# Performance work log

Measured on AMD Instinct MI355X. Metric: run time of the kernel, lower is better.

## Reference

```python
import jax, jax.numpy as jnp
import numpy as np

D_MODEL = 1024
NUM_HEADS = 16
HEAD_DIM = D_MODEL // NUM_HEADS
B, S = 2, 2048


def setup_inputs() -> dict:
    key = jax.random.key(0)
    ks = jax.random.split(key, 5)
    x = jax.random.normal(ks[0], (B, S, D_MODEL), dtype=jnp.float32)
    # nn.Linear weights are [out_features, in_features]
    Wq = jax.random.normal(ks[1], (D_MODEL, D_MODEL), dtype=jnp.float32) / np.sqrt(D_MODEL)
    Wk = jax.random.normal(ks[2], (HEAD_DIM, D_MODEL), dtype=jnp.float32) / np.sqrt(D_MODEL)
    Wv = jax.random.normal(ks[3], (HEAD_DIM, D_MODEL), dtype=jnp.float32) / np.sqrt(D_MODEL)
    Wo = jax.random.normal(ks[4], (D_MODEL, D_MODEL), dtype=jnp.float32) / np.sqrt(D_MODEL)
    # causal mask, broadcastable to [B, H, S, S]; mask==0 positions get -inf
    mask = jnp.tril(jnp.ones((S, S), dtype=bool))[None, None]
    return {"x": x, "Wq": Wq, "Wk": Wk, "Wv": Wv, "Wo": Wo, "mask": mask}


def reference(x, Wq, Wk, Wv, Wo, mask):
    Bsz, Sl, D = x.shape
    H, hd = NUM_HEADS, HEAD_DIM
    q = (x @ Wq.T).reshape(Bsz, Sl, H, hd)          # [B,S,H,hd]
    k = x @ Wk.T                                    # [B,S,hd] (single shared KV head)
    v = x @ Wv.T                                    # [B,S,hd]
    scale = 1.0 / np.sqrt(hd).astype(np.float32)
    # scores: [B,H,S,S] — full O(n^2) matrix, as in the original module
    scores = jnp.einsum('bshd,btd->bhst', q, k) * scale
    scores = jnp.where(mask, scores, -jnp.inf)
    attn = jax.nn.softmax(scores, axis=-1)
    out = jnp.einsum('bhst,btd->bshd', attn, v).reshape(Bsz, Sl, D)
    return out @ Wo.T
```

## Files before the change

### kernel.cpp

```cpp
#include <hip/hip_runtime.h>
#include <hip/hip_bf16.h>
#include <math.h>

#define BB 2
#define SS 2048
#define DD 1024
#define NH 16
#define HD 64
#define MM (BB * SS)

typedef __hip_bfloat16 bf16;
typedef __bf16 bf16_t;
typedef __attribute__((ext_vector_type(8))) __bf16 bf16x8;
typedef __attribute__((ext_vector_type(4))) __bf16 bf16x4;
typedef __attribute__((ext_vector_type(4))) float floatx4;

__global__ void detect_dtype(const unsigned int* __restrict__ x, int* __restrict__ flag) {
    const int tid = threadIdx.x;
    int good = 0;
    for (int i = tid; i < 256; i += 64) {
        unsigned int bits = (x[i] & 0xFFFFu) << 16;
        float v = __uint_as_float(bits);
        float av = fabsf(v);
        if (av == 0.f || (av >= 9.5367431640625e-7f && av <= 64.f)) good++;
    }
#pragma unroll
    for (int s = 1; s < 64; s <<= 1) good += __shfl_xor(good, s);
    if (tid == 0) *flag = (good >= 240) ? 0 : 1;
}

#define BK 32
#define KP 40

__device__ __forceinline__ bf16x4 cvt4(float4 v) {
    bf16x4 o;
    o[0] = (bf16_t)v.x; o[1] = (bf16_t)v.y; o[2] = (bf16_t)v.z; o[3] = (bf16_t)v.w;
    return o;
}

__global__ __launch_bounds__(256) void proj_qkv(const void* __restrict__ X,
                                                const void* __restrict__ Wq,
                                                const void* __restrict__ Wk,
                                                const void* __restrict__ Wv,
                                                bf16_t* __restrict__ QA,
                                                bf16_t* __restrict__ Kp,
                                                bf16_t* __restrict__ VpT,
                                                const int* __restrict__ flag) {
    const int f = *flag;

    __shared__ bf16_t As[128 * KP];
    __shared__ bf16_t Ws[128 * KP];

    const int tid = threadIdx.x;
    const int wave = tid >> 6, lane = tid & 63;
    const int lo = lane & 15, quad = lane >> 4;
    const int wr = wave >> 1, wc = wave & 1;
    const int cb = blockIdx.x;
    const int rowBase = blockIdx.y * 128;

    floatx4 acc[4][4];
#pragma unroll
    for (int i = 0; i < 4; i++)
#pragma unroll
        for (int j = 0; j < 4; j++) acc[i][j] = (floatx4){0.f, 0.f, 0.f, 0.f};

    if (f) {
        const int rA = tid >> 3, sg = tid & 7;
        const float* wrow[4];
        const float* arow[4];
#pragma unroll
        for (int p = 0; p < 4; p++) {
            int row = rA + 32 * p;
            arow[p] = (const float*)X + (size_t)(rowBase + row) * DD;
            if (cb < 8)        wrow[p] = (const float*)Wq + (size_t)(cb * 128 + row) * DD;
            else if (row < 64) wrow[p] = (const float*)Wk + (size_t)row * DD;
            else               wrow[p] = (const float*)Wv + (size_t)(row - 64) * DD;
        }
        float4 aR[4], wR[4];
#pragma unroll
        for (int p = 0; p < 4; p++) {
            aR[p] = *(const float4*)(arow[p] + sg * 4);
            wR[p] = *(const float4*)(wrow[p] + sg * 4);
        }
        for (int k0 = 0; k0 < DD; k0 += BK) {
            __syncthreads();
#pragma unroll
            for (int p = 0; p < 4; p++) {
                *(bf16x4*)&As[(rA + 32 * p) * KP + sg * 4] = cvt4(aR[p]);
                *(bf16x4*)&Ws[(rA + 32 * p) * KP + sg * 4] = cvt4(wR[p]);
            }
            __syncthreads();
            if (k0 + BK < DD) {
#pragma unroll
                for (int p = 0; p < 4; p++) {
                    aR[p] = *(const float4*)(arow[p] + k0 + BK + sg * 4);
                    wR[p] = *(const float4*)(wrow[p] + k0 + BK + sg * 4);
                }
            }
            bf16x8 afr[4], bfr[4];
#pragma unroll
            for (int i = 0; i < 4; i++)
                afr[i] = *(const bf16x8*)&As[(wr * 64 + i * 16 + lo) * KP + quad * 8];
#pragma unroll
            for (int j = 0; j < 4; j++)
                bfr[j] = *(const bf16x8*)&Ws[(wc * 64 + j * 16 + lo) * KP + quad * 8];
#pragma unroll
            for (int i = 0; i < 4; i++)
#pragma unroll
                for (int j = 0; j < 4; j++)
                    acc[i][j] = __builtin_amdgcn_mfma_f32_16x16x32_bf16(afr[i], bfr[j], acc[i][j], 0, 0, 0);
        }
    } else {
        const int rA = tid >> 2, sg = tid & 3;
        const bf16_t* arow[2];
        const bf16_t* wrow[2];
#pragma unroll
        for (int p = 0; p < 2; p++) {
            int row = rA + 64 * p;
            arow[p] = (const bf16_t*)X + (size_t)(rowBase + row) * DD;
            if (cb < 8)        wrow[p] = (const bf16_t*)Wq + (size_t)(cb * 128 + row) * DD;
            else if (row < 64) wrow[p] = (const bf16_t*)Wk + (size_t)row * DD;
            else               wrow[p] = (const bf16_t*)Wv + (size_t)(row - 64) * DD;
        }
        bf16x8 aR[2], wR[2];
#pragma unroll
        for (int p = 0; p < 2; p++) {
            aR[p] = *(const bf16x8*)(arow[p] + sg * 8);
            wR[p] = *(const bf16x8*)(wrow[p] + sg * 8);
        }
        for (int k0 = 0; k0 < DD; k0 += BK) {
            __syncthreads();
#pragma unroll
            for (int p = 0; p < 2; p++) {
                *(bf16x8*)&As[(rA + 64 * p) * KP + sg * 8] = aR[p];
                *(bf16x8*)&Ws[(rA + 64 * p) * KP + sg * 8] = wR[p];
            }
            __syncthreads();
            if (k0 + BK < DD) {
#pragma unroll
                for (int p = 0; p < 2; p++) {
                    aR[p] = *(const bf16x8*)(arow[p] + k0 + BK + sg * 8);
                    wR[p] = *(const bf16x8*)(wrow[p] + k0 + BK + sg * 8);
                }
            }
            bf16x8 afr[4], bfr[4];
#pragma unroll
            for (int i = 0; i < 4; i++)
                afr[i] = *(const bf16x8*)&As[(wr * 64 + i * 16 + lo) * KP + quad * 8];
#pragma unroll
            for (int j = 0; j < 4; j++)
                bfr[j] = *(const bf16x8*)&Ws[(wc * 64 + j * 16 + lo) * KP + quad * 8];
#pragma unroll
            for (int i = 0; i < 4; i++)
#pragma unroll
                for (int j = 0; j < 4; j++)
                    acc[i][j] = __builtin_amdgcn_mfma_f32_16x16x32_bf16(afr[i], bfr[j], acc[i][j], 0, 0, 0);
        }
    }

#pragma unroll
    for (int i = 0; i < 4; i++)
#pragma unroll
        for (int j = 0; j < 4; j++)
#pragma unroll
            for (int reg = 0; reg < 4; reg++) {
                int row = rowBase + wr * 64 + i * 16 + quad * 4 + reg;
                int col = wc * 64 + j * 16 + lo;
                bf16_t val = (bf16_t)acc[i][j][reg];
                if (cb < 8)         QA[(size_t)row * DD + cb * 128 + col] = val;
                else if (col < 64)  Kp[(size_t)row * HD + col] = val;
                else {
                    int d = col - 64;
                    VpT[((size_t)(row >> 11) * HD + d) * SS + (row & (SS - 1))] = val;
                }
            }
}

__global__ __launch_bounds__(256) void proj_o(const bf16_t* __restrict__ AO,
                                              const void* __restrict__ Wo,
                                              void* __restrict__ Cout,
                                              const int* __restrict__ flag) {
    const int f = *flag;

    __shared__ bf16_t As[128 * KP];
    __shared__ bf16_t Ws[128 * KP];

    const int tid = threadIdx.x;
    const int wave = tid >> 6, lane = tid & 63;
    const int lo = lane & 15, quad = lane >> 4;
    const int wr = wave >> 1, wc = wave & 1;
    const int colBase = blockIdx.x * 128;
    const int rowBase = blockIdx.y * 128;

    floatx4 acc[4][4];
#pragma unroll
    for (int i = 0; i < 4; i++)
#pragma unroll
        for (int j = 0; j < 4; j++) acc[i][j] = (floatx4){0.f, 0.f, 0.f, 0.f};

    const int rA = tid >> 2, sgA = tid & 3;
    const bf16_t* arow[2] = {AO + (size_t)(rowBase + rA) * DD,
                             AO + (size_t)(rowBase + rA + 64) * DD};
    bf16x8 aR[2];
#pragma unroll
    for (int p = 0; p < 2; p++) aR[p] = *(const bf16x8*)(arow[p] + sgA * 8);

    if (f) {
        const int rW = tid >> 3, sgW = tid & 7;
        const float* wrow[4];
#pragma unroll
        for (int p = 0; p < 4; p++)
            wrow[p] = (const float*)Wo + (size_t)(colBase + rW + 32 * p) * DD;
        float4 wR[4];
#pragma unroll
        for (int p = 0; p < 4; p++) wR[p] = *(const float4*)(wrow[p] + sgW * 4);

        for (int k0 = 0; k0 < DD; k0 += BK) {
            __syncthreads();
#pragma unroll
            for (int p = 0; p < 2; p++)
                *(bf16x8*)&As[(rA + 64 * p) * KP + sgA * 8] = aR[p];
#pragma unroll
            for (int p = 0; p < 4; p++)
                *(bf16x4*)&Ws[(rW + 32 * p) * KP + sgW * 4] = cvt4(wR[p]);
            __syncthreads();
            if (k0 + BK < DD) {
#pragma unroll
                for (int p = 0; p < 2; p++)
                    aR[p] = *(const bf16x8*)(arow[p] + k0 + BK + sgA * 8);
#pragma unroll
                for (int p = 0; p < 4; p++)
                    wR[p] = *(const float4*)(wrow[p] + k0 + BK + sgW * 4);
            }
            bf16x8 afr[4], bfr[4];
#pragma unroll
            for (int i = 0; i < 4; i++)
                afr[i] = *(const bf16x8*)&As[(wr * 64 + i * 16 + lo) * KP + quad * 8];
#pragma unroll
            for (int j = 0; j < 4; j++)
                bfr[j] = *(const bf16x8*)&Ws[(wc * 64 + j * 16 + lo) * KP + quad * 8];
#pragma unroll
            for (int i = 0; i < 4; i++)
#pragma unroll
                for (int j = 0; j < 4; j++)
                    acc[i][j] = __builtin_amdgcn_mfma_f32_16x16x32_bf16(afr[i], bfr[j], acc[i][j], 0, 0, 0);
        }
    } else {
        const int rW = tid >> 2, sgW = tid & 3;
        const bf16_t* wrow[2];
#pragma unroll
        for (int p = 0; p < 2; p++)
            wrow[p] = (const bf16_t*)Wo + (size_t)(colBase + rW + 64 * p) * DD;
        bf16x8 wR[2];
#pragma unroll
        for (int p = 0; p < 2; p++) wR[p] = *(const bf16x8*)(wrow[p] + sgW * 8);

        for (int k0 = 0; k0 < DD; k0 += BK) {
            __syncthreads();
#pragma unroll
            for (int p = 0; p < 2; p++) {
                *(bf16x8*)&As[(rA + 64 * p) * KP + sgA * 8] = aR[p];
                *(bf16x8*)&Ws[(rW + 64 * p) * KP + sgW * 8] = wR[p];
            }
            __syncthreads();
            if (k0 + BK < DD) {
#pragma unroll
                for (int p = 0; p < 2; p++) {
                    aR[p] = *(const bf16x8*)(arow[p] + k0 + BK + sgA * 8);
                    wR[p] = *(const bf16x8*)(wrow[p] + k0 + BK + sgW * 8);
                }
            }
            bf16x8 afr[4], bfr[4];
#pragma unroll
            for (int i = 0; i < 4; i++)
                afr[i] = *(const bf16x8*)&As[(wr * 64 + i * 16 + lo) * KP + quad * 8];
#pragma unroll
            for (int j = 0; j < 4; j++)
                bfr[j] = *(const bf16x8*)&Ws[(wc * 64 + j * 16 + lo) * KP + quad * 8];
#pragma unroll
            for (int i = 0; i < 4; i++)
#pragma unroll
                for (int j = 0; j < 4; j++)
                    acc[i][j] = __builtin_amdgcn_mfma_f32_16x16x32_bf16(afr[i], bfr[j], acc[i][j], 0, 0, 0);
        }
    }

#pragma unroll
    for (int i = 0; i < 4; i++)
#pragma unroll
        for (int j = 0; j < 4; j++)
#pragma unroll
            for (int reg = 0; reg < 4; reg++) {
                int row = rowBase + wr * 64 + i * 16 + quad * 4 + reg;
                int col = colBase + wc * 64 + j * 16 + lo;
                size_t idx = (size_t)row * DD + col;
                if (f) ((float*)Cout)[idx] = acc[i][j][reg];
                else   ((bf16_t*)Cout)[idx] = (bf16_t)acc[i][j][reg];
            }
}

#define PSTR 40
#define ALOG2E 0.18033688011112042f

__global__ __launch_bounds__(256) void attn_mfma(const bf16_t* Q,
                                                 const bf16_t* __restrict__ K,
                                                 const bf16_t* __restrict__ Vt,
                                                 bf16_t* O) {
    const int h = blockIdx.y, b = blockIdx.z;
    const int tid = threadIdx.x;
    const int wq = tid >> 6, lane = tid & 63;
    const int lo = lane & 15, quad = lane >> 4;
    const int x = blockIdx.x;
    const int qt = (wq & 1) ? (31 + (wq >> 1) * 32 - x) : ((wq >> 1) * 32 + x);
    const int q0 = qt * 32;

    __shared__ bf16_t Ps[4][32 * PSTR];
    bf16_t* Pw = Ps[wq];

    bf16x8 qf[2][2];
#pragma unroll
    for (int s = 0; s < 2; s++)
#pragma unroll
        for (int hf = 0; hf < 2; hf++)
            qf[s][hf] = *(const bf16x8*)(Q + ((size_t)(b * SS + q0 + s * 16 + lo)) * DD +
                                         h * HD + hf * 32 + quad * 8);

    floatx4 Oacc[2][4];
    float m_i[2], l_i[2];
#pragma unroll
    for (int s = 0; s < 2; s++) {
#pragma unroll
        for (int dt = 0; dt < 4; dt++) Oacc[s][dt] = (floatx4){0.f, 0.f, 0.f, 0.f};
        m_i[s] = -1e30f; l_i[s] = 0.f;
    }

    const bf16_t* Kb = K + (size_t)b * SS * HD;
    const bf16_t* Vb = Vt + (size_t)b * HD * SS;

    bf16x8 kf[2][2];
#pragma unroll
    for (int kt = 0; kt < 2; kt++)
#pragma unroll
        for (int hf = 0; hf < 2; hf++)
            kf[kt][hf] = *(const bf16x8*)(Kb + (size_t)(kt * 16 + lo) * HD + hf * 32 + quad * 8);

    for (int it = 0; it <= qt; it++) {
        const int t0 = it * 32;

        bf16x8 vf[4];
#pragma unroll
        for (int dt = 0; dt < 4; dt++)
            vf[dt] = *(const bf16x8*)(Vb + (size_t)(dt * 16 + lo) * SS + t0 + quad * 8);

        bf16x8 kn[2][2];
        if (it < qt) {
#pragma unroll
            for (int kt = 0; kt < 2; kt++)
#pragma unroll
                for (int hf = 0; hf < 2; hf++)
                    kn[kt][hf] = *(const bf16x8*)(Kb + (size_t)(t0 + 32 + kt * 16 + lo) * HD +
                                                  hf * 32 + quad * 8);
        }

        floatx4 st[2][2];
#pragma unroll
        for (int s = 0; s < 2; s++)
#pragma unroll
            for (int kt = 0; kt < 2; kt++) {
                floatx4 z = (floatx4){0.f, 0.f, 0.f, 0.f};
                z = __builtin_amdgcn_mfma_f32_16x16x32_bf16(kf[kt][0], qf[s][0], z, 0, 0, 0);
                z = __builtin_amdgcn_mfma_f32_16x16x32_bf16(kf[kt][1], qf[s][1], z, 0, 0, 0);
                st[s][kt] = z;
            }

        if (it == qt) {
#pragma unroll
            for (int s = 0; s < 2; s++) {
                int q = q0 + s * 16 + lo;
#pragma unroll
                for (int kt = 0; kt < 2; kt++)
#pragma unroll
                    for (int reg = 0; reg < 4; reg++)
                        if (t0 + kt * 16 + quad * 4 + reg > q) st[s][kt][reg] = -1e30f;
            }
        }

#pragma unroll
        for (int s = 0; s < 2; s++) {
            float mx = fmaxf(fmaxf(fmaxf(st[s][0][0], st[s][0][1]), fmaxf(st[s][0][2], st[s][0][3])),
                             fmaxf(fmaxf(st[s][1][0], st[s][1][1]), fmaxf(st[s][1][2], st[s][1][3])));
            mx = fmaxf(mx, __shfl_xor(mx, 16));
            mx = fmaxf(mx, __shfl_xor(mx, 32));
            float mn = fmaxf(m_i[s], mx);
            float al = exp2f((m_i[s] - mn) * ALOG2E);
            m_i[s] = mn;
            float mnA = mn * ALOG2E;
            float p[2][4];
#pragma unroll
            for (int kt = 0; kt < 2; kt++)
#pragma unroll
                for (int reg = 0; reg < 4; reg++)
                    p[kt][reg] = exp2f(st[s][kt][reg] * ALOG2E - mnA);
            float rs = ((p[0][0] + p[0][1]) + (p[0][2] + p[0][3])) +
                       ((p[1][0] + p[1][1]) + (p[1][2] + p[1][3]));
            rs += __shfl_xor(rs, 16);
            rs += __shfl_xor(rs, 32);
            l_i[s] = l_i[s] * al + rs;
#pragma unroll
            for (int kt = 0; kt < 2; kt++) {
                bf16x4 pk;
#pragma unroll
                for (int reg = 0; reg < 4; reg++) pk[reg] = (bf16_t)p[kt][reg];
                *(bf16x4*)&Pw[(s * 16 + lo) * PSTR + kt * 16 + quad * 4] = pk;
            }
#pragma unroll
            for (int dt = 0; dt < 4; dt++) Oacc[s][dt] *= al;
        }

        asm volatile("s_waitcnt lgkmcnt(0)" ::: "memory");

        bf16x8 pb[2];
#pragma unroll
        for (int s = 0; s < 2; s++)
            pb[s] = *(const bf16x8*)&Pw[(s * 16 + lo) * PSTR + quad * 8];
#pragma unroll
        for (int s = 0; s < 2; s++)
#pragma unroll
            for (int dt = 0; dt < 4; dt++)
                Oacc[s][dt] = __builtin_amdgcn_mfma_f32_16x16x32_bf16(vf[dt], pb[s], Oacc[s][dt], 0, 0, 0);

#pragma unroll
        for (int kt = 0; kt < 2; kt++)
#pragma unroll
            for (int hf = 0; hf < 2; hf++) kf[kt][hf] = kn[kt][hf];
    }

#pragma unroll
    for (int s = 0; s < 2; s++) {
        float inv = 1.f / l_i[s];
        bf16_t* Orow = O + ((size_t)(b * SS + q0 + s * 16 + lo)) * DD + h * HD;
#pragma unroll
        for (int dt = 0; dt < 4; dt++) {
            bf16x4 ov;
#pragma unroll
            for (int reg = 0; reg < 4; reg++) ov[reg] = (bf16_t)(Oacc[s][dt][reg] * inv);
            *(bf16x4*)&Orow[dt * 16 + quad * 4] = ov;
        }
    }
}

extern "C" void kernel_launch(void* const* d_in, const int* in_sizes, int n_in,
                              void* d_out, int out_size, void* d_ws, size_t ws_size,
                              hipStream_t stream) {
    const void* x  = d_in[0];
    const void* Wq = d_in[1];
    const void* Wk = d_in[2];
    const void* Wv = d_in[3];
    const void* Wo = d_in[4];

    char* ws = (char*)d_ws;
    int* flag = (int*)ws;
    bf16_t* QA  = (bf16_t*)(ws + 256);
    bf16_t* Kp  = QA + (size_t)MM * DD;
    bf16_t* VpT = Kp + (size_t)MM * HD;

    detect_dtype<<<1, 64, 0, stream>>>((const unsigned int*)x, flag);

    proj_qkv<<<dim3(9, MM / 128), dim3(256), 0, stream>>>(x, Wq, Wk, Wv, QA, Kp, VpT, flag);

    attn_mfma<<<dim3(SS / 32 / 4, NH, BB), dim3(256), 0, stream>>>(QA, Kp, VpT, QA);

    proj_o<<<dim3(DD / 128, MM / 128), dim3(256), 0, stream>>>(QA, Wo, d_out, flag);
}
```

Measured before the change: 226.1 us.

## Split attention KV range across wave pairs and shrink GEMM tiles for more blocks

The attention kernel now gives each pair of waves one query tile and splits its causal KV range in half. The two partial softmax states are merged through shared memory, which doubles the grid and balances work per wave. The projection GEMMs move from 128x128 to 128x64 output tiles so they launch twice as many blocks, which helps fill the CUs. The cost is lower data reuse per block in the GEMMs, extra shared memory in attention, and a block-wide sync for the merge.

Measured after the change: 210.7 us. 6.8% less time.

```diff
diff --git a/kernel.cpp b/kernel.cpp
--- a/kernel.cpp
+++ b/kernel.cpp
@@ -49,63 +49,65 @@
     const int f = *flag;
 
     __shared__ bf16_t As[128 * KP];
-    __shared__ bf16_t Ws[128 * KP];
+    __shared__ bf16_t Ws[64 * KP];
 
     const int tid = threadIdx.x;
     const int wave = tid >> 6, lane = tid & 63;
     const int lo = lane & 15, quad = lane >> 4;
-    const int wr = wave >> 1, wc = wave & 1;
+    const int rb = wave * 32;
     const int cb = blockIdx.x;
     const int rowBase = blockIdx.y * 128;
 
-    floatx4 acc[4][4];
-#pragma unroll
-    for (int i = 0; i < 4; i++)
+    floatx4 acc[2][4];
+#pragma unroll
+    for (int i = 0; i < 2; i++)
 #pragma unroll
         for (int j = 0; j < 4; j++) acc[i][j] = (floatx4){0.f, 0.f, 0.f, 0.f};
 
     if (f) {
         const int rA = tid >> 3, sg = tid & 7;
-        const float* wrow[4];
         const float* arow[4];
-#pragma unroll
-        for (int p = 0; p < 4; p++) {
+        const float* wrow[2];
+#pragma unroll
+        for (int p = 0; p < 4; p++)
+            arow[p] = (const float*)X + (size_t)(rowBase + rA + 32 * p) * DD;
+#pragma unroll
+        for (int p = 0; p < 2; p++) {
             int row = rA + 32 * p;
-            arow[p] = (const float*)X + (size_t)(rowBase + row) * DD;
-            if (cb < 8)        wrow[p] = (const float*)Wq + (size_t)(cb * 128 + row) * DD;
-            else if (row < 64) wrow[p] = (const float*)Wk + (size_t)row * DD;
-            else               wrow[p] = (const float*)Wv + (size_t)(row - 64) * DD;
-        }
-        float4 aR[4], wR[4];
-#pragma unroll
-        for (int p = 0; p < 4; p++) {
-            aR[p] = *(const float4*)(arow[p] + sg * 4);
-            wR[p] = *(const float4*)(wrow[p] + sg * 4);
-        }
+            if (cb < 16)       wrow[p] = (const float*)Wq + (size_t)(cb * 64 + row) * DD;
+            else if (cb == 16) wrow[p] = (const float*)Wk + (size_t)row * DD;
+            else               wrow[p] = (const float*)Wv + (size_t)row * DD;
+        }
+        float4 aR[4], wR[2];
+#pragma unroll
+        for (int p = 0; p < 4; p++) aR[p] = *(const float4*)(arow[p] + sg * 4);
+#pragma unroll
+        for (int p = 0; p < 2; p++) wR[p] = *(const float4*)(wrow[p] + sg * 4);
+
         for (int k0 = 0; k0 < DD; k0 += BK) {
             __syncthreads();
 #pragma unroll
-            for (int p = 0; p < 4; p++) {
+            for (int p = 0; p < 4; p++)
                 *(bf16x4*)&As[(rA + 32 * p) * KP + sg * 4] = cvt4(aR[p]);
+#pragma unroll
+            for (int p = 0; p < 2; p++)
                 *(bf16x4*)&Ws[(rA + 32 * p) * KP + sg * 4] = cvt4(wR[p]);
-            }
             __syncthreads();
             if (k0 + BK < DD) {
 #pragma unroll
-                for (int p = 0; p < 4; p++) {
-                    aR[p] = *(const float4*)(arow[p] + k0 + BK + sg * 4);
-                    wR[p] = *(const float4*)(wrow[p] + k0 + BK + sg * 4);
-                }
-            }
-            bf16x8 afr[4], bfr[4];
-#pragma unroll
-            for (int i = 0; i < 4; i++)
-                afr[i] = *(const bf16x8*)&As[(wr * 64 + i * 16 + lo) * KP + quad * 8];
+                for (int p = 0; p < 4; p++) aR[p] = *(const float4*)(arow[p] + k0 + BK + sg * 4);
+#pragma unroll
+                for (int p = 0; p < 2; p++) wR[p] = *(const float4*)(wrow[p] + k0 + BK + sg * 4);
+            }
+            bf16x8 afr[2], bfr[4];
+#pragma unroll
+            for (int i = 0; i < 2; i++)
+                afr[i] = *(const bf16x8*)&As[(rb + i * 16 + lo) * KP + quad * 8];
 #pragma unroll
             for (int j = 0; j < 4; j++)
-                bfr[j] = *(const bf16x8*)&Ws[(wc * 64 + j * 16 + lo) * KP + quad * 8];
-#pragma unroll
-            for (int i = 0; i < 4; i++)
+                bfr[j] = *(const bf16x8*)&Ws[(j * 16 + lo) * KP + quad * 8];
+#pragma unroll
+            for (int i = 0; i < 2; i++)
 #pragma unroll
                 for (int j = 0; j < 4; j++)
                     acc[i][j] = __builtin_amdgcn_mfma_f32_16x16x32_bf16(afr[i], bfr[j], acc[i][j], 0, 0, 0);
@@ -113,45 +115,39 @@
     } else {
         const int rA = tid >> 2, sg = tid & 3;
         const bf16_t* arow[2];
-        const bf16_t* wrow[2];
-#pragma unroll
-        for (int p = 0; p < 2; p++) {
-            int row = rA + 64 * p;
-            arow[p] = (const bf16_t*)X + (size_t)(rowBase + row) * DD;
-            if (cb < 8)        wrow[p] = (const bf16_t*)Wq + (size_t)(cb * 128 + row) * DD;
-            else if (row < 64) wrow[p] = (const bf16_t*)Wk + (size_t)row * DD;
-            else               wrow[p] = (const bf16_t*)Wv + (size_t)(row - 64) * DD;
-        }
-        bf16x8 aR[2], wR[2];
-#pragma unroll
-        for (int p = 0; p < 2; p++) {
-            aR[p] = *(const bf16x8*)(arow[p] + sg * 8);
-            wR[p] = *(const bf16x8*)(wrow[p] + sg * 8);
-        }
+        const bf16_t* wrow;
+#pragma unroll
+        for (int p = 0; p < 2; p++)
+            arow[p] = (const bf16_t*)X + (size_t)(rowBase + rA + 64 * p) * DD;
+        if (cb < 16)       wrow = (const bf16_t*)Wq + (size_t)(cb * 64 + rA) * DD;
+        else if (cb == 16) wrow = (const bf16_t*)Wk + (size_t)rA * DD;
+        else               wrow = (const bf16_t*)Wv + (size_t)rA * DD;
+        bf16x8 aR[2], wR;
+#pragma unroll
+        for (int p = 0; p < 2; p++) aR[p] = *(const bf16x8*)(arow[p] + sg * 8);
+        wR = *(const bf16x8*)(wrow + sg * 8);
+
         for (int k0 = 0; k0 < DD; k0 += BK) {
             __syncthreads();
 #pragma unroll
-            for (int p = 0; p < 2; p++) {
+            for (int p = 0; p < 2; p++)
                 *(bf16x8*)&As[(rA + 64 * p) * KP + sg * 8] = aR[p];
-                *(bf16x8*)&Ws[(rA + 64 * p) * KP + sg * 8] = wR[p];
-            }
+            *(bf16x8*)&Ws[rA * KP + sg * 8] = wR;
             __syncthreads();
             if (k0 + BK < DD) {
 #pragma unroll
-                for (int p = 0; p < 2; p++) {
-                    aR[p] = *(const bf16x8*)(arow[p] + k0 + BK + sg * 8);
-                    wR[p] = *(const bf16x8*)(wrow[p] + k0 + BK + sg * 8);
-                }
-            }
-            bf16x8 afr[4], bfr[4];
-#pragma unroll
-            for (int i = 0; i < 4; i++)
-                afr[i] = *(const bf16x8*)&As[(wr * 64 + i * 16 + lo) * KP + quad * 8];
+                for (int p = 0; p < 2; p++) aR[p] = *(const bf16x8*)(arow[p] + k0 + BK + sg * 8);
+                wR = *(const bf16x8*)(wrow + k0 + BK + sg * 8);
+            }
+            bf16x8 afr[2], bfr[4];
+#pragma unroll
+            for (int i = 0; i < 2; i++)
+                afr[i] = *(const bf16x8*)&As[(rb + i * 16 + lo) * KP + quad * 8];
 #pragma unroll
             for (int j = 0; j < 4; j++)
-                bfr[j] = *(const bf16x8*)&Ws[(wc * 64 + j * 16 + lo) * KP + quad * 8];
-#pragma unroll
-            for (int i = 0; i < 4; i++)
+                bfr[j] = *(const bf16x8*)&Ws[(j * 16 + lo) * KP + quad * 8];
+#pragma unroll
+            for (int i = 0; i < 2; i++)
 #pragma unroll
                 for (int j = 0; j < 4; j++)
                     acc[i][j] = __builtin_amdgcn_mfma_f32_16x16x32_bf16(afr[i], bfr[j], acc[i][j], 0, 0, 0);
@@ -159,20 +155,17 @@
     }
 
 #pragma unroll
-    for (int i = 0; i < 4; i++)
+    for (int i = 0; i < 2; i++)
 #pragma unroll
         for (int j = 0; j < 4; j++)
 #pragma unroll
             for (int reg = 0; reg < 4; reg++) {
-                int row = rowBase + wr * 64 + i * 16 + quad * 4 + reg;
-                int col = wc * 64 + j * 16 + lo;
+                int row = rowBase + rb + i * 16 + quad * 4 + reg;
+                int col = j * 16 + lo;
                 bf16_t val = (bf16_t)acc[i][j][reg];
-                if (cb < 8)         QA[(size_t)row * DD + cb * 128 + col] = val;
-                else if (col < 64)  Kp[(size_t)row * HD + col] = val;
-                else {
-                    int d = col - 64;
-                    VpT[((size_t)(row >> 11) * HD + d) * SS + (row & (SS - 1))] = val;
-                }
+                if (cb < 16)       QA[(size_t)row * DD + cb * 64 + col] = val;
+                else if (cb == 16) Kp[(size_t)row * HD + col] = val;
+                else               VpT[((size_t)(row >> 11) * HD + col) * SS + (row & (SS - 1))] = val;
             }
 }
 
@@ -183,102 +176,91 @@
     const int f = *flag;
 
     __shared__ bf16_t As[128 * KP];
-    __shared__ bf16_t Ws[128 * KP];
+    __shared__ bf16_t Ws[64 * KP];
 
     const int tid = threadIdx.x;
     const int wave = tid >> 6, lane = tid & 63;
     const int lo = lane & 15, quad = lane >> 4;
-    const int wr = wave >> 1, wc = wave & 1;
-    const int colBase = blockIdx.x * 128;
+    const int rb = wave * 32;
+    const int colBase = blockIdx.x * 64;
     const int rowBase = blockIdx.y * 128;
 
-    floatx4 acc[4][4];
-#pragma unroll
-    for (int i = 0; i < 4; i++)
+    floatx4 acc[2][4];
+#pragma unroll
+    for (int i = 0; i < 2; i++)
 #pragma unroll
         for (int j = 0; j < 4; j++) acc[i][j] = (floatx4){0.f, 0.f, 0.f, 0.f};
 
-    const int rA = tid >> 2, sgA = tid & 3;
-    const bf16_t* arow[2] = {AO + (size_t)(rowBase + rA) * DD,
-                             AO + (size_t)(rowBase + rA + 64) * DD};
+    const int rA2 = tid >> 2, sgA = tid & 3;
+    const bf16_t* arow[2] = {AO + (size_t)(rowBase + rA2) * DD,
+                             AO + (size_t)(rowBase + rA2 + 64) * DD};
     bf16x8 aR[2];
 #pragma unroll
     for (int p = 0; p < 2; p++) aR[p] = *(const bf16x8*)(arow[p] + sgA * 8);
 
     if (f) {
         const int rW = tid >> 3, sgW = tid & 7;
-        const float* wrow[4];
-#pragma unroll
-        for (int p = 0; p < 4; p++)
+        const float* wrow[2];
+#pragma unroll
+        for (int p = 0; p < 2; p++)
             wrow[p] = (const float*)Wo + (size_t)(colBase + rW + 32 * p) * DD;
-        float4 wR[4];
-#pragma unroll
-        for (int p = 0; p < 4; p++) wR[p] = *(const float4*)(wrow[p] + sgW * 4);
+        float4 wR[2];
+#pragma unroll
+        for (int p = 0; p < 2; p++) wR[p] = *(const float4*)(wrow[p] + sgW * 4);
 
         for (int k0 = 0; k0 < DD; k0 += BK) {
             __syncthreads();
 #pragma unroll
             for (int p = 0; p < 2; p++)
-                *(bf16x8*)&As[(rA + 64 * p) * KP + sgA * 8] = aR[p];
-#pragma unroll
-            for (int p = 0; p < 4; p++)
+                *(bf16x8*)&As[(rA2 + 64 * p) * KP + sgA * 8] = aR[p];
+#pragma unroll
+            for (int p = 0; p < 2; p++)
                 *(bf16x4*)&Ws[(rW + 32 * p) * KP + sgW * 4] = cvt4(wR[p]);
             __syncthreads();
             if (k0 + BK < DD) {
 #pragma unroll
-                for (int p = 0; p < 2; p++)
-                    aR[p] = *(const bf16x8*)(arow[p] + k0 + BK + sgA * 8);
-#pragma unroll
-                for (int p = 0; p < 4; p++)
-                    wR[p] = *(const float4*)(wrow[p] + k0 + BK + sgW * 4);
-            }
-            bf16x8 afr[4], bfr[4];
-#pragma unroll
-            for (int i = 0; i < 4; i++)
-                afr[i] = *(const bf16x8*)&As[(wr * 64 + i * 16 + lo) * KP + quad * 8];
+                for (int p = 0; p < 2; p++) aR[p] = *(const bf16x8*)(arow[p] + k0 + BK + sgA * 8);
+#pragma unroll
+                for (int p = 0; p < 2; p++) wR[p] = *(const float4*)(wrow[p] + k0 + BK + sgW * 4);
+            }
+            bf16x8 afr[2], bfr[4];
+#pragma unroll
+            for (int i = 0; i < 2; i++)
+                afr[i] = *(const bf16x8*)&As[(rb + i * 16 + lo) * KP + quad * 8];
 #pragma unroll
             for (int j = 0; j < 4; j++)
-                bfr[j] = *(const bf16x8*)&Ws[(wc * 64 + j * 16 + lo) * KP + quad * 8];
-#pragma unroll
-            for (int i = 0; i < 4; i++)
+                bfr[j] = *(const bf16x8*)&Ws[(j * 16 + lo) * KP + quad * 8];
+#pragma unroll
+            for (int i = 0; i < 2; i++)
 #pragma unroll
                 for (int j = 0; j < 4; j++)
                     acc[i][j] = __builtin_amdgcn_mfma_f32_16x16x32_bf16(afr[i], bfr[j], acc[i][j], 0, 0, 0);
         }
     } else {
-        const int rW = tid >> 2, sgW = tid & 3;
-        const bf16_t* wrow[2];
-#pragma unroll
-        for (int p = 0; p < 2; p++)
-            wrow[p] = (const bf16_t*)Wo + (size_t)(colBase + rW + 64 * p) * DD;
-        bf16x8 wR[2];
-#pragma unroll
-        for (int p = 0; p < 2; p++) wR[p] = *(const bf16x8*)(wrow[p] + sgW * 8);
+        const bf16_t* wrow = (const bf16_t*)Wo + (size_t)(colBase + rA2) * DD;
+        bf16x8 wR = *(const bf16x8*)(wrow + sgA * 8);
 
         for (int k0 = 0; k0 < DD; k0 += BK) {
             __syncthreads();
 #pragma unroll
-            for (int p = 0; p < 2; p++) {
-                *(bf16x8*)&As[(rA + 64 * p) * KP + sgA * 8] = aR[p];
-                *(bf16x8*)&Ws[(rW + 64 * p) * KP + sgW * 8] = wR[p];
-            }
+            for (int p = 0; p < 2; p++)
+                *(bf16x8*)&As[(rA2 + 64 * p) * KP + sgA * 8] = aR[p];
+            *(bf16x8*)&Ws[rA2 * KP + sgA * 8] = wR;
             __syncthreads();
             if (k0 + BK < DD) {
 #pragma unroll
-                for (int p = 0; p < 2; p++) {
-                    aR[p] = *(const bf16x8*)(arow[p] + k0 + BK + sgA * 8);
-                    wR[p] = *(const bf16x8*)(wrow[p] + k0 + BK + sgW * 8);
-                }
-            }
-            bf16x8 afr[4], bfr[4];
-#pragma unroll
-            for (int i = 0; i < 4; i++)
-                afr[i] = *(const bf16x8*)&As[(wr * 64 + i * 16 + lo) * KP + quad * 8];
+                for (int p = 0; p < 2; p++) aR[p] = *(const bf16x8*)(arow[p] + k0 + BK + sgA * 8);
+                wR = *(const bf16x8*)(wrow + k0 + BK + sgA * 8);
+            }
+            bf16x8 afr[2], bfr[4];
+#pragma unroll
+            for (int i = 0; i < 2; i++)
+                afr[i] = *(const bf16x8*)&As[(rb + i * 16 + lo) * KP + quad * 8];
 #pragma unroll
             for (int j = 0; j < 4; j++)
-                bfr[j] = *(const bf16x8*)&Ws[(wc * 64 + j * 16 + lo) * KP + quad * 8];
-#pragma unroll
-            for (int i = 0; i < 4; i++)
+                bfr[j] = *(const bf16x8*)&Ws[(j * 16 + lo) * KP + quad * 8];
+#pragma unroll
+            for (int i = 0; i < 2; i++)
 #pragma unroll
                 for (int j = 0; j < 4; j++)
                     acc[i][j] = __builtin_amdgcn_mfma_f32_16x16x32_bf16(afr[i], bfr[j], acc[i][j], 0, 0, 0);
@@ -286,13 +268,13 @@
     }
 
 #pragma unroll
-    for (int i = 0; i < 4; i++)
+    for (int i = 0; i < 2; i++)
 #pragma unroll
         for (int j = 0; j < 4; j++)
 #pragma unroll
             for (int reg = 0; reg < 4; reg++) {
-                int row = rowBase + wr * 64 + i * 16 + quad * 4 + reg;
-                int col = colBase + wc * 64 + j * 16 + lo;
+                int row = rowBase + rb + i * 16 + quad * 4 + reg;
+                int col = colBase + j * 16 + lo;
                 size_t idx = (size_t)row * DD + col;
                 if (f) ((float*)Cout)[idx] = acc[i][j][reg];
                 else   ((bf16_t*)Cout)[idx] = (bf16_t)acc[i][j][reg];
@@ -302,19 +284,27 @@
 #define PSTR 40
 #define ALOG2E 0.18033688011112042f
 
-__global__ __launch_bounds__(256) void attn_mfma(const bf16_t* Q,
-                                                 const bf16_t* __restrict__ K,
-                                                 const bf16_t* __restrict__ Vt,
-                                                 bf16_t* O) {
+__global__ __launch_bounds__(256, 4) void attn_mfma(const bf16_t* Q,
+                                                    const bf16_t* __restrict__ K,
+                                                    const bf16_t* __restrict__ Vt,
+                                                    bf16_t* O) {
     const int h = blockIdx.y, b = blockIdx.z;
     const int tid = threadIdx.x;
     const int wq = tid >> 6, lane = tid & 63;
     const int lo = lane & 15, quad = lane >> 4;
     const int x = blockIdx.x;
-    const int qt = (wq & 1) ? (31 + (wq >> 1) * 32 - x) : ((wq >> 1) * 32 + x);
+    const int pr = wq >> 1;
+    const int hh = wq & 1;
+    const int qt = pr ? (63 - x) : x;
     const int q0 = qt * 32;
+    const int nt = qt + 1;
+    const int nt0 = nt >> 1;
+    const int itS = hh ? nt0 : 0;
+    const int itE = hh ? nt : nt0;
 
     __shared__ bf16_t Ps[4][32 * PSTR];
+    __shared__ float MrgO[2][32][64];
+    __shared__ float MrgML[2][2][2][16];
     bf16_t* Pw = Ps[wq];
 
     bf16x8 qf[2][2];
@@ -337,114 +327,142 @@
     const bf16_t* Kb = K + (size_t)b * SS * HD;
     const bf16_t* Vb = Vt + (size_t)b * HD * SS;
 
-    bf16x8 kf[2][2];
-#pragma unroll
-    for (int kt = 0; kt < 2; kt++)
-#pragma unroll
-        for (int hf = 0; hf < 2; hf++)
-            kf[kt][hf] = *(const bf16x8*)(Kb + (size_t)(kt * 16 + lo) * HD + hf * 32 + quad * 8);
-
-    for (int it = 0; it <= qt; it++) {
-        const int t0 = it * 32;
-
-        bf16x8 vf[4];
-#pragma unroll
-        for (int dt = 0; dt < 4; dt++)
-            vf[dt] = *(const bf16x8*)(Vb + (size_t)(dt * 16 + lo) * SS + t0 + quad * 8);
-
-        bf16x8 kn[2][2];
-        if (it < qt) {
+    if (itS < itE) {
+        bf16x8 kf[2][2];
+#pragma unroll
+        for (int kt = 0; kt < 2; kt++)
+#pragma unroll
+            for (int hf = 0; hf < 2; hf++)
+                kf[kt][hf] = *(const bf16x8*)(Kb + (size_t)(itS * 32 + kt * 16 + lo) * HD +
+                                              hf * 32 + quad * 8);
+
+        for (int it = itS; it < itE; it++) {
+            const int t0 = it * 32;
+
+            bf16x8 vf[4];
+#pragma unroll
+            for (int dt = 0; dt < 4; dt++)
+                vf[dt] = *(const bf16x8*)(Vb + (size_t)(dt * 16 + lo) * SS + t0 + quad * 8);
+
+            bf16x8 kn[2][2];
+            if (it + 1 < itE) {
+#pragma unroll
+                for (int kt = 0; kt < 2; kt++)
+#pragma unroll
+                    for (int hf = 0; hf < 2; hf++)
+                        kn[kt][hf] = *(const bf16x8*)(Kb + (size_t)(t0 + 32 + kt * 16 + lo) * HD +
+                                                      hf * 32 + quad * 8);
+            }
+
+            floatx4 st[2][2];
+#pragma unroll
+            for (int s = 0; s < 2; s++)
+#pragma unroll
+                for (int kt = 0; kt < 2; kt++) {
+                    floatx4 z = (floatx4){0.f, 0.f, 0.f, 0.f};
+                    z = __builtin_amdgcn_mfma_f32_16x16x32_bf16(kf[kt][0], qf[s][0], z, 0, 0, 0);
+                    z = __builtin_amdgcn_mfma_f32_16x16x32_bf16(kf[kt][1], qf[s][1], z, 0, 0, 0);
+                    st[s][kt] = z;
+                }
+
+            if (it == qt) {
+#pragma unroll
+                for (int s = 0; s < 2; s++) {
+                    int q = q0 + s * 16 + lo;
+#pragma unroll
+                    for (int kt = 0; kt < 2; kt++)
+#pragma unroll
+                        for (int reg = 0; reg < 4; reg++)
+                            if (t0 + kt * 16 + quad * 4 + reg > q) st[s][kt][reg] = -1e30f;
+                }
+            }
+
+#pragma unroll
+            for (int s = 0; s < 2; s++) {
+                float mx = fmaxf(fmaxf(fmaxf(st[s][0][0], st[s][0][1]), fmaxf(st[s][0][2], st[s][0][3])),
+                                 fmaxf(fmaxf(st[s][1][0], st[s][1][1]), fmaxf(st[s][1][2], st[s][1][3])));
+                mx = fmaxf(mx, __shfl_xor(mx, 16));
+                mx = fmaxf(mx, __shfl_xor(mx, 32));
+                float mn = fmaxf(m_i[s], mx);
+                float al = exp2f((m_i[s] - mn) * ALOG2E);
+                m_i[s] = mn;
+                float mnA = mn * ALOG2E;
+                float p[2][4];
+#pragma unroll
+                for (int kt = 0; kt < 2; kt++)
+#pragma unroll
+                    for (int reg = 0; reg < 4; reg++)
+                        p[kt][reg] = exp2f(st[s][kt][reg] * ALOG2E - mnA);
+                float rs = ((p[0][0] + p[0][1]) + (p[0][2] + p[0][3])) +
+                           ((p[1][0] + p[1][1]) + (p[1][2] + p[1][3]));
+                rs += __shfl_xor(rs, 16);
+                rs += __shfl_xor(rs, 32);
+                l_i[s] = l_i[s] * al + rs;
+#pragma unroll
+                for (int kt = 0; kt < 2; kt++) {
+                    bf16x4 pk;
+#pragma unroll
+                    for (int reg = 0; reg < 4; reg++) pk[reg] = (bf16_t)p[kt][reg];
+                    *(bf16x4*)&Pw[(s * 16 + lo) * PSTR + kt * 16 + quad * 4] = pk;
+                }
+#pragma unroll
+                for (int dt = 0; dt < 4; dt++) Oacc[s][dt] *= al;
+            }
+
+            asm volatile("s_waitcnt lgkmcnt(0)" ::: "memory");
+
+            bf16x8 pb[2];
+#pragma unroll
+            for (int s = 0; s < 2; s++)
+                pb[s] = *(const bf16x8*)&Pw[(s * 16 + lo) * PSTR + quad * 8];
+#pragma unroll
+            for (int s = 0; s < 2; s++)
+#pragma unroll
+                for (int dt = 0; dt < 4; dt++)
+                    Oacc[s][dt] = __builtin_amdgcn_mfma_f32_16x16x32_bf16(vf[dt], pb[s], Oacc[s][dt], 0, 0, 0);
+
 #pragma unroll
             for (int kt = 0; kt < 2; kt++)
 #pragma unroll
-                for (int hf = 0; hf < 2; hf++)
-                    kn[kt][hf] = *(const bf16x8*)(Kb + (size_t)(t0 + 32 + kt * 16 + lo) * HD +
-                                                  hf * 32 + quad * 8);
-        }
-
-        floatx4 st[2][2];
-#pragma unroll
-        for (int s = 0; s < 2; s++)
-#pragma unroll
-            for (int kt = 0; kt < 2; kt++) {
-                floatx4 z = (floatx4){0.f, 0.f, 0.f, 0.f};
-                z = __builtin_amdgcn_mfma_f32_16x16x32_bf16(kf[kt][0], qf[s][0], z, 0, 0, 0);
-                z = __builtin_amdgcn_mfma_f32_16x16x32_bf16(kf[kt][1], qf[s][1], z, 0, 0, 0);
-                st[s][kt] = z;
-            }
-
-        if (it == qt) {
-#pragma unroll
-            for (int s = 0; s < 2; s++) {
-                int q = q0 + s * 16 + lo;
-#pragma unroll
-                for (int kt = 0; kt < 2; kt++)
-#pragma unroll
-                    for (int reg = 0; reg < 4; reg++)
-                        if (t0 + kt * 16 + quad * 4 + reg > q) st[s][kt][reg] = -1e30f;
-            }
-        }
-
+                for (int hf = 0; hf < 2; hf++) kf[kt][hf] = kn[kt][hf];
+        }
+    }
+
+    if (hh) {
 #pragma unroll
         for (int s = 0; s < 2; s++) {
-            float mx = fmaxf(fmaxf(fmaxf(st[s][0][0], st[s][0][1]), fmaxf(st[s][0][2], st[s][0][3])),
-                             fmaxf(fmaxf(st[s][1][0], st[s][1][1]), fmaxf(st[s][1][2], st[s][1][3])));
-            mx = fmaxf(mx, __shfl_xor(mx, 16));
-            mx = fmaxf(mx, __shfl_xor(mx, 32));
-            float mn = fmaxf(m_i[s], mx);
-            float al = exp2f((m_i[s] - mn) * ALOG2E);
-            m_i[s] = mn;
-            float mnA = mn * ALOG2E;
-            float p[2][4];
-#pragma unroll
-            for (int kt = 0; kt < 2; kt++)
+#pragma unroll
+            for (int dt = 0; dt < 4; dt++)
 #pragma unroll
                 for (int reg = 0; reg < 4; reg++)
-                    p[kt][reg] = exp2f(st[s][kt][reg] * ALOG2E - mnA);
-            float rs = ((p[0][0] + p[0][1]) + (p[0][2] + p[0][3])) +
-                       ((p[1][0] + p[1][1]) + (p[1][2] + p[1][3]));
-            rs += __shfl_xor(rs, 16);
-            rs += __shfl_xor(rs, 32);
-            l_i[s] = l_i[s] * al + rs;
-#pragma unroll
-            for (int kt = 0; kt < 2; kt++) {
-                bf16x4 pk;
-#pragma unroll
-                for (int reg = 0; reg < 4; reg++) pk[reg] = (bf16_t)p[kt][reg];
-                *(bf16x4*)&Pw[(s * 16 + lo) * PSTR + kt * 16 + quad * 4] = pk;
-            }
-#pragma unroll
-            for (int dt = 0; dt < 4; dt++) Oacc[s][dt] *= al;
-        }
-
-        asm volatile("s_waitcnt lgkmcnt(0)" ::: "memory");
-
-        bf16x8 pb[2];
-#pragma unroll
-        for (int s = 0; s < 2; s++)
-            pb[s] = *(const bf16x8*)&Pw[(s * 16 + lo) * PSTR + quad * 8];
-#pragma unroll
-        for (int s = 0; s < 2; s++)
-#pragma unroll
-            for (int dt = 0; dt < 4; dt++)
-                Oacc[s][dt] = __builtin_amdgcn_mfma_f32_16x16x32_bf16(vf[dt], pb[s], Oacc[s][dt], 0, 0, 0);
-
-#pragma unroll
-        for (int kt = 0; kt < 2; kt++)
-#pragma unroll
-            for (int hf = 0; hf < 2; hf++) kf[kt][hf] = kn[kt][hf];
-    }
-
-#pragma unroll
-    for (int s = 0; s < 2; s++) {
-        float inv = 1.f / l_i[s];
-        bf16_t* Orow = O + ((size_t)(b * SS + q0 + s * 16 + lo)) * DD + h * HD;
-#pragma unroll
-        for (int dt = 0; dt < 4; dt++) {
-            bf16x4 ov;
-#pragma unroll
-            for (int reg = 0; reg < 4; reg++) ov[reg] = (bf16_t)(Oacc[s][dt][reg] * inv);
-            *(bf16x4*)&Orow[dt * 16 + quad * 4] = ov;
+                    MrgO[pr][s * 16 + dt * 4 + reg][lane] = Oacc[s][dt][reg];
+            if (quad == 0) {
+                MrgML[pr][s][0][lo] = m_i[s];
+                MrgML[pr][s][1][lo] = l_i[s];
+            }
+        }
+    }
+    __syncthreads();
+    if (!hh) {
+#pragma unroll
+        for (int s = 0; s < 2; s++) {
+            float m1 = MrgML[pr][s][0][lo];
+            float l1 = MrgML[pr][s][1][lo];
+            float mm = fmaxf(m_i[s], m1);
+            float a0 = exp2f((m_i[s] - mm) * ALOG2E);
+            float a1 = exp2f((m1 - mm) * ALOG2E);
+            float linv = 1.f / (l_i[s] * a0 + l1 * a1);
+            bf16_t* Orow = O + ((size_t)(b * SS + q0 + s * 16 + lo)) * DD + h * HD;
+#pragma unroll
+            for (int dt = 0; dt < 4; dt++) {
+                bf16x4 ov;
+#pragma unroll
+                for (int reg = 0; reg < 4; reg++) {
+                    float o1 = MrgO[pr][s * 16 + dt * 4 + reg][lane];
+                    ov[reg] = (bf16_t)((Oacc[s][dt][reg] * a0 + o1 * a1) * linv);
+                }
+                *(bf16x4*)&Orow[dt * 16 + quad * 4] = ov;
+            }
         }
     }
 }
@@ -466,9 +484,9 @@
 
     detect_dtype<<<1, 64, 0, stream>>>((const unsigned int*)x, flag);
 
-    proj_qkv<<<dim3(9, MM / 128), dim3(256), 0, stream>>>(x, Wq, Wk, Wv, QA, Kp, VpT, flag);
-
-    attn_mfma<<<dim3(SS / 32 / 4, NH, BB), dim3(256), 0, stream>>>(QA, Kp, VpT, QA);
-
-    proj_o<<<dim3(DD / 128, MM / 128), dim3(256), 0, stream>>>(QA, Wo, d_out, flag);
-}
+    proj_qkv<<<dim3(18, MM / 128), dim3(256), 0, stream>>>(x, Wq, Wk, Wv, QA, Kp, VpT, flag);
+
+    attn_mfma<<<dim3(32, NH, BB), dim3(256), 0, stream>>>(QA, Kp, VpT, QA);
+
+    proj_o<<<dim3(16, MM / 128), dim3(256), 0, stream>>>(QA, Wo, d_out, flag);
+}
```
